# Kernel tuning notes

Measured on AMD Instinct MI355X. Metric: run time of the kernel, lower is better.

Reference implementation:

```python
import jax, jax.numpy as jnp
import numpy as np

HID, HEADS, FF, DEPTH = 1152, 16, 4304, 2
HD = HID // HEADS            # 72
ROT = HD // 2                # 36 (rotary_pos_emb width)
S, NSEG = 2048, 4
EPS = 1e-6


def _layernorm(x, w, b):
    m = jnp.mean(x, axis=-1, keepdims=True)
    xc = x - m
    v = jnp.mean(xc * xc, axis=-1, keepdims=True)
    return xc * jax.lax.rsqrt(v + EPS) * w + b


def _rotate_half(x):
    x1, x2 = jnp.split(x, 2, axis=-1)
    return jnp.concatenate([-x2, x1], axis=-1)


def _apply_rotary(t, freqs):
    # t: [S, H, D], freqs: [S, D/2]
    emb = jnp.concatenate([freqs, freqs], axis=-1)          # [S, D]
    cos = jnp.cos(emb)[:, None, :]
    sin = jnp.sin(emb)[:, None, :]
    return t * cos + _rotate_half(t) * sin


def setup_inputs() -> dict:
    key = jax.random.key(0)
    ks = jax.random.split(key, 16)
    sd = 0.02
    # rotary freqs as in VisionRotaryEmbedding(dim=HD//2): h-pos and w-pos halves
    inv_freq = 1.0 / (10000.0 ** (jnp.arange(0, ROT, 2, dtype=jnp.float32) / ROT))  # [18]
    pos = jnp.arange(S, dtype=jnp.float32)
    hpos, wpos = pos // 32.0, pos % 32.0
    rotary = jnp.concatenate([jnp.outer(hpos, inv_freq), jnp.outer(wpos, inv_freq)], axis=-1)  # [S, 36]
    return {
        "x": jax.random.normal(ks[0], (S, HID), jnp.float32),
        "cu_seqlens": jnp.arange(NSEG + 1, dtype=jnp.int32) * (S // NSEG),
        "rotary_pos_emb": rotary,
        "norm1_w": jnp.ones((DEPTH, HID), jnp.float32),
        "norm1_b": jnp.zeros((DEPTH, HID), jnp.float32),
        "qkv_w": jax.random.normal(ks[1], (DEPTH, 3 * HID, HID), jnp.float32) * sd,
        "qkv_b": jnp.zeros((DEPTH, 3 * HID), jnp.float32),
        "proj_w": jax.random.normal(ks[2], (DEPTH, HID, HID), jnp.float32) * sd,
        "proj_b": jnp.zeros((DEPTH, HID), jnp.float32),
        "norm2_w": jnp.ones((DEPTH, HID), jnp.float32),
        "norm2_b": jnp.zeros((DEPTH, HID), jnp.float32),
        "fc1_w": jax.random.normal(ks[3], (DEPTH, FF, HID), jnp.float32) * sd,
        "fc1_b": jnp.zeros((DEPTH, FF), jnp.float32),
        "fc2_w": jax.random.normal(ks[4], (DEPTH, HID, FF), jnp.float32) * sd,
        "fc2_b": jnp.zeros((DEPTH, HID), jnp.float32),
    }


def _forward(x, cu_seqlens, rotary_pos_emb, norm1_w, norm1_b, qkv_w, qkv_b,
             proj_w, proj_b, norm2_w, norm2_b, fc1_w, fc1_b, fc2_w, fc2_b):
    seq_len = x.shape[0]
    # block-diagonal additive mask from cu_seqlens (same mask the torch loop builds)
    seg = jnp.searchsorted(cu_seqlens, jnp.arange(seq_len, dtype=cu_seqlens.dtype), side="right") - 1
    same = seg[:, None] == seg[None, :]
    bias = jnp.where(same, jnp.float32(0.0), jnp.finfo(jnp.float32).min)  # [S, S]
    scale = 1.0 / np.sqrt(HD)
    for d in range(DEPTH):
        # --- attention ---
        h = _layernorm(x, norm1_w[d], norm1_b[d])
        qkv = (h @ qkv_w[d].T + qkv_b[d]).reshape(seq_len, 3, HEADS, HD)
        q, k, v = qkv[:, 0], qkv[:, 1], qkv[:, 2]           # [S, H, D]
        q = _apply_rotary(q, rotary_pos_emb)
        k = _apply_rotary(k, rotary_pos_emb)
        scores = jnp.einsum("qhd,khd->hqk", q, k) * scale + bias[None]
        probs = jax.nn.softmax(scores.astype(jnp.float32), axis=-1).astype(q.dtype)
        attn = jnp.einsum("hqk,khd->qhd", probs, v).reshape(seq_len, HID)
        x = x + attn @ proj_w[d].T + proj_b[d]
        # --- MLP (gelu tanh approx) ---
        h2 = _layernorm(x, norm2_w[d], norm2_b[d])
        x = x + jax.nn.gelu(h2 @ fc1_w[d].T + fc1_b[d], approximate=True) @ fc2_w[d].T + fc2_b[d]
    return x


def reference(x, cu_seqlens, rotary_pos_emb, norm1_w, norm1_b, qkv_w, qkv_b,
              proj_w, proj_b, norm2_w, norm2_b, fc1_w, fc1_b, fc2_w, fc2_b):
    return _forward(x, cu_seqlens, rotary_pos_emb, norm1_w, norm1_b, qkv_w, qkv_b,
                    proj_w, proj_b, norm2_w, norm2_b, fc1_w, fc1_b, fc2_w, fc2_b)
```

## Files before the change

kernel.cpp:

```cpp
#include <hip/hip_runtime.h>

#define S_LEN 2048
#define HID   1152
#define HEADS 16
#define HD    72
#define ROT   36
#define LD3   3456
#define FF    4304
#define FFP   4320

typedef short s16x8 __attribute__((ext_vector_type(8)));
typedef short s16x4 __attribute__((ext_vector_type(4)));
typedef float f32x4 __attribute__((ext_vector_type(4)));
typedef short bf_t;

__device__ __forceinline__ short f2b(float f) {
  unsigned u = __float_as_uint(f);
  u += 0x7fffu + ((u >> 16) & 1u);
  return (short)(u >> 16);
}
__device__ __forceinline__ float b2f(short h) {
  return __uint_as_float(((unsigned)(unsigned short)h) << 16);
}
__device__ __forceinline__ float gelu_f(float x) {
  float t = tanhf(0.7978845608028654f * (x + 0.044715f * x * x * x));
  return 0.5f * x * (1.0f + t);
}

typedef const __attribute__((address_space(1))) void* gas_p;
typedef __attribute__((address_space(3))) void* las_p;
__device__ __forceinline__ void gload16(const void* g, void* l) {
  __builtin_amdgcn_global_load_lds((gas_p)g, (las_p)l, 16, 0, 0);
}

__global__ __launch_bounds__(256) void convw4_kernel(
    const float* __restrict__ src, int N, int K,
    bf_t* __restrict__ dst, int Kpad)
{
  int idx = blockIdx.x * 256 + threadIdx.x;
  int kq = Kpad >> 2;
  if (idx >= N * kq) return;
  int n = idx / kq, k = (idx % kq) << 2;
  s16x4 o;
  if (k + 3 < K) {
    float4 v = *(const float4*)(src + (size_t)n * K + k);
    o[0] = f2b(v.x); o[1] = f2b(v.y); o[2] = f2b(v.z); o[3] = f2b(v.w);
  } else {
#pragma unroll
    for (int j = 0; j < 4; j++) {
      int kk = k + j;
      o[j] = (kk < K) ? f2b(src[(size_t)n * K + kk]) : (short)0;
    }
  }
  *(s16x4*)(dst + (size_t)n * Kpad + k) = o;
}

__global__ __launch_bounds__(256) void costab_kernel(
    const float* __restrict__ rot, float* __restrict__ ct, float* __restrict__ st)
{
  int i = blockIdx.x * 256 + threadIdx.x;
  if (i < S_LEN * ROT) { float f = rot[i]; ct[i] = cosf(f); st[i] = sinf(f); }
}

__global__ __launch_bounds__(256) void ln_kernel(
    const float* __restrict__ x, const float* __restrict__ wgt,
    const float* __restrict__ bia, bf_t* __restrict__ outb)
{
  const int row = blockIdx.x, tid = threadIdx.x;
  const float4* xr = (const float4*)(x + (size_t)row * HID);
  float4 a = xr[tid];
  float4 b2 = make_float4(0.f, 0.f, 0.f, 0.f);
  const bool has2 = tid < 32;
  if (has2) b2 = xr[256 + tid];
  float s = a.x + a.y + a.z + a.w + b2.x + b2.y + b2.z + b2.w;
  float q = a.x*a.x + a.y*a.y + a.z*a.z + a.w*a.w
          + b2.x*b2.x + b2.y*b2.y + b2.z*b2.z + b2.w*b2.w;
  for (int mk = 32; mk; mk >>= 1) { s += __shfl_xor(s, mk); q += __shfl_xor(q, mk); }
  __shared__ float red[16];
  if ((tid & 63) == 0) { red[tid >> 6] = s; red[8 + (tid >> 6)] = q; }
  __syncthreads();
  if (tid == 0) {
    red[4]  = red[0] + red[1] + red[2] + red[3];
    red[12] = red[8] + red[9] + red[10] + red[11];
  }
  __syncthreads();
  float mean = red[4] * (1.0f / HID);
  float var  = red[12] * (1.0f / HID) - mean * mean;
  float rstd = rsqrtf(var + 1e-6f);
  const float4* w4 = (const float4*)wgt;
  const float4* b4 = (const float4*)bia;
  s16x4* o4 = (s16x4*)(outb + (size_t)row * HID);
  {
    float4 wv = w4[tid], bv = b4[tid];
    s16x4 o;
    o[0] = f2b((a.x - mean) * rstd * wv.x + bv.x);
    o[1] = f2b((a.y - mean) * rstd * wv.y + bv.y);
    o[2] = f2b((a.z - mean) * rstd * wv.z + bv.z);
    o[3] = f2b((a.w - mean) * rstd * wv.w + bv.w);
    o4[tid] = o;
  }
  if (has2) {
    float4 wv = w4[256 + tid], bv = b4[256 + tid];
    s16x4 o;
    o[0] = f2b((b2.x - mean) * rstd * wv.x + bv.x);
    o[1] = f2b((b2.y - mean) * rstd * wv.y + bv.y);
    o[2] = f2b((b2.z - mean) * rstd * wv.z + bv.z);
    o[3] = f2b((b2.w - mean) * rstd * wv.w + bv.w);
    o4[256 + tid] = o;
  }
}

__global__ __launch_bounds__(256) void rotary_kernel(
    bf_t* __restrict__ qkv, const float* __restrict__ ct, const float* __restrict__ st)
{
  int idx = blockIdx.x * 256 + threadIdx.x;
  if (idx >= S_LEN * HEADS * ROT) return;
  int t = idx / (HEADS * ROT);
  int r = idx % (HEADS * ROT);
  int h = r / ROT, dd = r % ROT;
  float c = ct[t * ROT + dd], s = st[t * ROT + dd];
  size_t base = (size_t)t * LD3 + h * HD + dd;
  float q1 = b2f(qkv[base]),        q2 = b2f(qkv[base + ROT]);
  float k1 = b2f(qkv[base + HID]),  k2 = b2f(qkv[base + HID + ROT]);
  const float scale = 0.11785113019775793f;
  qkv[base]             = f2b((q1 * c - q2 * s) * scale);
  qkv[base + ROT]       = f2b((q2 * c + q1 * s) * scale);
  qkv[base + HID]       = f2b(k1 * c - k2 * s);
  qkv[base + HID + ROT] = f2b(k2 * c + k1 * s);
}

template<int MODE>
__global__ __launch_bounds__(256, 4) void gemm_bt(
    const bf_t* __restrict__ A, int lda,
    const bf_t* __restrict__ B, int ldb,
    const float* __restrict__ bias, int nbias,
    void* outp, int ldc, int nvalid, int K, int kchunk)
{
  __shared__ __align__(16) bf_t As[128 * 32];
  __shared__ __align__(16) bf_t Bs[128 * 32];
  const int tid = threadIdx.x;
  const int l = tid & 63, w = tid >> 6;
  const int lr = l & 15, lg = l >> 4;
  const int wm = (w >> 1) * 64, wn = (w & 1) * 64;

  unsigned gx = gridDim.x, gy = gridDim.y, gz = gridDim.z;
  unsigned nwg = gx * gy * gz;
  unsigned lin = (blockIdx.z * gy + blockIdx.y) * gx + blockIdx.x;
  if ((nwg & 7u) == 0u) {
    unsigned q = nwg >> 3;
    lin = (lin & 7u) * q + (lin >> 3);
  }
  const unsigned bz = lin / (gx * gy);
  const unsigned rem = lin % (gx * gy);
  const unsigned by = rem / gx, bx = rem % gx;

  const int rowA0 = by * 128, colB0 = bx * 128;
  const int kb0 = bz * kchunk;
  int kb1 = kb0 + kchunk; if (kb1 > K) kb1 = K;

  const int o1 = tid * 16, o2 = o1 + 4096;
  const int r1 = o1 >> 6, c1 = o1 & 63;
  const int r2 = o2 >> 6, c2 = o2 & 63;
  const char* Ab = (const char*)A;
  const char* Bb = (const char*)B;

  f32x4 acc[4][4] = {};

  for (int kb = kb0; kb < kb1; kb += 32) {
    gload16(Ab + ((size_t)(rowA0 + r1) * lda + kb) * 2 + c1, (char*)As + o1);
    gload16(Ab + ((size_t)(rowA0 + r2) * lda + kb) * 2 + c2, (char*)As + o2);
    gload16(Bb + ((size_t)(colB0 + r1) * ldb + kb) * 2 + c1, (char*)Bs + o1);
    gload16(Bb + ((size_t)(colB0 + r2) * ldb + kb) * 2 + c2, (char*)Bs + o2);
    asm volatile("s_waitcnt vmcnt(0)" ::: "memory");
    __syncthreads();
    s16x8 af[4], bv[4];
#pragma unroll
    for (int mt = 0; mt < 4; mt++) af[mt] = *(const s16x8*)&As[(wm + mt * 16 + lr) * 32 + lg * 8];
#pragma unroll
    for (int nt = 0; nt < 4; nt++) bv[nt] = *(const s16x8*)&Bs[(wn + nt * 16 + lr) * 32 + lg * 8];
#pragma unroll
    for (int mt = 0; mt < 4; mt++)
#pragma unroll
      for (int nt = 0; nt < 4; nt++)
        acc[mt][nt] = __builtin_amdgcn_mfma_f32_16x16x32_bf16(af[mt], bv[nt], acc[mt][nt], 0, 0, 0);
    __syncthreads();
  }

#pragma unroll
  for (int mt = 0; mt < 4; mt++) {
    const int rr = rowA0 + wm + mt * 16 + lg * 4;
#pragma unroll
    for (int nt = 0; nt < 4; nt++) {
      const int cc = colB0 + wn + nt * 16 + lr;
      const float bvl = (cc < nbias) ? bias[cc] : 0.0f;
#pragma unroll
      for (int i = 0; i < 4; i++) {
        float v = acc[mt][nt][i] + bvl;
        const int row = rr + i;
        if (MODE == 0) {
          ((bf_t*)outp)[(size_t)row * ldc + cc] = f2b(v);
        } else if (MODE == 2) {
          if (cc < nvalid)      ((bf_t*)outp)[(size_t)row * ldc + cc] = f2b(gelu_f(v));
          else if (cc < ldc)    ((bf_t*)outp)[(size_t)row * ldc + cc] = 0;
        } else {
          float* P = (float*)outp + (size_t)bz * ((size_t)S_LEN * ldc);
          P[(size_t)row * ldc + cc] = v;
        }
      }
    }
  }
}

__global__ __launch_bounds__(256) void reduce_kernel(
    const float* __restrict__ part, const float* __restrict__ bias,
    const float* __restrict__ resid, float* __restrict__ outp)
{
  int idx = blockIdx.x * 256 + threadIdx.x;
  if (idx >= S_LEN * HID / 4) return;
  float4 r = ((const float4*)resid)[idx];
  float4 bv = ((const float4*)bias)[idx % (HID / 4)];
  float sx = r.x + bv.x, sy = r.y + bv.y, sz = r.z + bv.z, sw = r.w + bv.w;
#pragma unroll
  for (int p = 0; p < 4; p++) {
    float4 v = ((const float4*)(part + (size_t)p * S_LEN * HID))[idx];
    sx += v.x; sy += v.y; sz += v.z; sw += v.w;
  }
  ((float4*)outp)[idx] = make_float4(sx, sy, sz, sw);
}

#define QSTR 104
#define VSTR 72
#define PSTR 72
__global__ __launch_bounds__(256, 2) void attn_kernel(
    const bf_t* __restrict__ qkv, const int* __restrict__ cu, int nseg,
    bf_t* __restrict__ outb)
{
  __shared__ __align__(16) bf_t Qs[64 * QSTR];
  __shared__ __align__(16) bf_t Ks[64 * QSTR];
  __shared__ __align__(16) bf_t VTs[80 * VSTR];
  __shared__ __align__(16) bf_t Pb[4][16 * PSTR];
  const int tid = threadIdx.x;
  const int l = tid & 63, w = tid >> 6;
  const int lr = l & 15, lg = l >> 4;
  const int h = blockIdx.y;
  const int qbase = blockIdx.x * 64;

  int kstart = 0, kend = S_LEN;
  for (int s2 = 0; s2 < nseg; s2++) {
    int a = cu[s2], b = cu[s2 + 1];
    if (qbase >= a && qbase < b) { kstart = a; kend = b; }
  }

  for (int i = tid; i < 64 * QSTR; i += 256)
    if ((i % QSTR) >= HD) { Qs[i] = 0; Ks[i] = 0; }
  for (int i = tid; i < 80 * VSTR; i += 256)
    if ((i / VSTR) >= HD) VTs[i] = 0;
  for (int c = tid; c < 576; c += 256) {
    int r = c / 9, j = c % 9;
    *(s16x8*)&Qs[r * QSTR + j * 8] =
        *(const s16x8*)&qkv[(size_t)(qbase + r) * LD3 + h * HD + j * 8];
  }
  __syncthreads();
  s16x8 qf[3];
#pragma unroll
  for (int ks = 0; ks < 3; ks++)
    qf[ks] = *(const s16x8*)&Qs[(w * 16 + lr) * QSTR + ks * 32 + lg * 8];

  float m_i[4], l_i[4];
  f32x4 Of[5] = {};
#pragma unroll
  for (int i = 0; i < 4; i++) { m_i[i] = -1e30f; l_i[i] = 0.0f; }

  for (int kb = kstart; kb < kend; kb += 64) {
    __syncthreads();
    for (int c = tid; c < 576; c += 256) {
      int r = c / 9, j = c % 9;
      int gr = kb + r; if (gr >= kend) gr = kend - 1;
      *(s16x8*)&Ks[r * QSTR + j * 8] =
          *(const s16x8*)&qkv[(size_t)gr * LD3 + HID + h * HD + j * 8];
    }
    for (int c = tid; c < 576; c += 256) {
      int r = c / 9, j = c % 9;
      int gr = kb + r; if (gr >= kend) gr = kend - 1;
      s16x8 v = *(const s16x8*)&qkv[(size_t)gr * LD3 + 2 * HID + h * HD + j * 8];
#pragma unroll
      for (int jj = 0; jj < 8; jj++) VTs[(j * 8 + jj) * VSTR + r] = v[jj];
    }
    __syncthreads();

    f32x4 sc[4] = {};
#pragma unroll
    for (int kc = 0; kc < 4; kc++) {
#pragma unroll
      for (int ks = 0; ks < 3; ks++) {
        s16x8 kf = *(const s16x8*)&Ks[(kc * 16 + lr) * QSTR + ks * 32 + lg * 8];
        sc[kc] = __builtin_amdgcn_mfma_f32_16x16x32_bf16(qf[ks], kf, sc[kc], 0, 0, 0);
      }
    }
#pragma unroll
    for (int kc = 0; kc < 4; kc++) {
      if ((kb + kc * 16 + lr) >= kend) {
#pragma unroll
        for (int i = 0; i < 4; i++) sc[kc][i] = -1e30f;
      }
    }
    float tmax[4], scl[4], rs[4];
#pragma unroll
    for (int i = 0; i < 4; i++) {
      float t = fmaxf(fmaxf(sc[0][i], sc[1][i]), fmaxf(sc[2][i], sc[3][i]));
#pragma unroll
      for (int d2 = 1; d2 < 16; d2 <<= 1) t = fmaxf(t, __shfl_xor(t, d2));
      tmax[i] = t;
    }
#pragma unroll
    for (int i = 0; i < 4; i++) {
      float mn = fmaxf(m_i[i], tmax[i]);
      scl[i] = __expf(m_i[i] - mn);
      m_i[i] = mn;
      rs[i] = 0.0f;
    }
#pragma unroll
    for (int kc = 0; kc < 4; kc++)
#pragma unroll
      for (int i = 0; i < 4; i++) {
        float p = __expf(sc[kc][i] - m_i[i]);
        sc[kc][i] = p;
        rs[i] += p;
      }
#pragma unroll
    for (int i = 0; i < 4; i++) {
#pragma unroll
      for (int d2 = 1; d2 < 16; d2 <<= 1) rs[i] += __shfl_xor(rs[i], d2);
      l_i[i] = l_i[i] * scl[i] + rs[i];
    }
#pragma unroll
    for (int nt = 0; nt < 5; nt++)
#pragma unroll
      for (int i = 0; i < 4; i++) Of[nt][i] *= scl[i];
#pragma unroll
    for (int kc = 0; kc < 4; kc++)
#pragma unroll
      for (int i = 0; i < 4; i++)
        Pb[w][(lg * 4 + i) * PSTR + kc * 16 + lr] = f2b(sc[kc][i]);
    __syncthreads();
    s16x8 pf[2];
#pragma unroll
    for (int k2 = 0; k2 < 2; k2++)
      pf[k2] = *(const s16x8*)&Pb[w][lr * PSTR + k2 * 32 + lg * 8];
#pragma unroll
    for (int nt = 0; nt < 5; nt++) {
#pragma unroll
      for (int k2 = 0; k2 < 2; k2++) {
        s16x8 vf = *(const s16x8*)&VTs[(nt * 16 + lr) * VSTR + k2 * 32 + lg * 8];
        Of[nt] = __builtin_amdgcn_mfma_f32_16x16x32_bf16(pf[k2], vf, Of[nt], 0, 0, 0);
      }
    }
  }
  float inv[4];
#pragma unroll
  for (int i = 0; i < 4; i++) inv[i] = 1.0f / l_i[i];
#pragma unroll
  for (int nt = 0; nt < 5; nt++) {
    int cc = nt * 16 + lr;
    if (cc < HD) {
#pragma unroll
      for (int i = 0; i < 4; i++) {
        int row = qbase + w * 16 + lg * 4 + i;
        outb[(size_t)row * HID + h * HD + cc] = f2b(Of[nt][i] * inv[i]);
      }
    }
  }
}

extern "C" void kernel_launch(void* const* d_in, const int* in_sizes, int n_in,
                              void* d_out, int out_size, void* d_ws, size_t ws_size,
                              hipStream_t stream) {
  const float* x     = (const float*)d_in[0];
  const int*   cu    = (const int*)d_in[1];
  const float* rotab = (const float*)d_in[2];
  const float* n1w   = (const float*)d_in[3];
  const float* n1b   = (const float*)d_in[4];
  const float* qkvw  = (const float*)d_in[5];
  const float* qkvb  = (const float*)d_in[6];
  const float* projw = (const float*)d_in[7];
  const float* projb = (const float*)d_in[8];
  const float* n2w   = (const float*)d_in[9];
  const float* n2b   = (const float*)d_in[10];
  const float* fc1w  = (const float*)d_in[11];
  const float* fc1b  = (const float*)d_in[12];
  const float* fc2w  = (const float*)d_in[13];
  const float* fc2b  = (const float*)d_in[14];
  float* out = (float*)d_out;
  char* ws = (char*)d_ws;

  size_t off = 0;
  float* xbuf = (float*)(ws + off); off += (size_t)S_LEN * HID * 4;
  bf_t* hbf   = (bf_t*)(ws + off);  off += (size_t)S_LEN * HID * 2;
  bf_t* qkvbf = (bf_t*)(ws + off);
  bf_t* ff1bf = (bf_t*)(ws + off);  off += (size_t)S_LEN * FFP * 2;
  bf_t* attnbf= (bf_t*)(ws + off);  off += (size_t)S_LEN * HID * 2;
  bf_t* wslot = (bf_t*)(ws + off);  off += (size_t)4352 * 1152 * 2;
  float* ctab = (float*)(ws + off); off += (size_t)S_LEN * ROT * 4;
  float* stab = (float*)(ws + off); off += (size_t)S_LEN * ROT * 4;
  float* part = (float*)(ws + off); off += (size_t)4 * S_LEN * HID * 4;

  hipMemcpyAsync(xbuf, x, (size_t)S_LEN * HID * 4, hipMemcpyDeviceToDevice, stream);
  costab_kernel<<<(S_LEN * ROT + 255) / 256, 256, 0, stream>>>(rotab, ctab, stab);

  const int nseg = in_sizes[1] - 1;
  const int RED_GRID = (S_LEN * HID / 4 + 255) / 256;

  for (int d = 0; d < 2; d++) {
    ln_kernel<<<S_LEN, 256, 0, stream>>>(xbuf, n1w + d * HID, n1b + d * HID, hbf);
    convw4_kernel<<<(LD3 * HID / 4 + 255) / 256, 256, 0, stream>>>(
        qkvw + (size_t)d * LD3 * HID, LD3, HID, wslot, HID);
    gemm_bt<0><<<dim3(LD3 / 128, 16), 256, 0, stream>>>(
        hbf, HID, wslot, HID, qkvb + (size_t)d * LD3, LD3, qkvbf, LD3, LD3, HID, HID);
    rotary_kernel<<<(S_LEN * HEADS * ROT + 255) / 256, 256, 0, stream>>>(qkvbf, ctab, stab);
    attn_kernel<<<dim3(S_LEN / 64, HEADS), 256, 0, stream>>>(qkvbf, cu, nseg, attnbf);
    convw4_kernel<<<(HID * HID / 4 + 255) / 256, 256, 0, stream>>>(
        projw + (size_t)d * HID * HID, HID, HID, wslot, HID);
    gemm_bt<3><<<dim3(HID / 128, 16, 4), 256, 0, stream>>>(
        attnbf, HID, wslot, HID, nullptr, 0, part, HID, HID, HID, 288);
    reduce_kernel<<<RED_GRID, 256, 0, stream>>>(part, projb + (size_t)d * HID, xbuf, xbuf);
    ln_kernel<<<S_LEN, 256, 0, stream>>>(xbuf, n2w + d * HID, n2b + d * HID, hbf);
    convw4_kernel<<<(FF * HID / 4 + 255) / 256, 256, 0, stream>>>(
        fc1w + (size_t)d * FF * HID, FF, HID, wslot, HID);
    gemm_bt<2><<<dim3(4352 / 128, 16), 256, 0, stream>>>(
        hbf, HID, wslot, HID, fc1b + (size_t)d * FF, FF, ff1bf, FFP, FF, HID, HID);
    convw4_kernel<<<(HID * FFP / 4 + 255) / 256, 256, 0, stream>>>(
        fc2w + (size_t)d * HID * FF, HID, FF, wslot, FFP);
    gemm_bt<3><<<dim3(HID / 128, 16, 4), 256, 0, stream>>>(
        ff1bf, FFP, wslot, FFP, nullptr, 0, part, HID, HID, FFP, 1088);
    float* outp = (d == 1) ? out : xbuf;
    reduce_kernel<<<RED_GRID, 256, 0, stream>>>(part, fc2b + (size_t)d * HID, xbuf, outp);
  }
}
```

Baseline: 461.4 us.

## Double-buffer GEMM shared tiles and shrink N tile to 64

```diff
diff --git a/kernel.cpp b/kernel.cpp
--- a/kernel.cpp
+++ b/kernel.cpp
@@ -136,12 +136,12 @@
     const float* __restrict__ bias, int nbias,
     void* outp, int ldc, int nvalid, int K, int kchunk)
 {
-  __shared__ __align__(16) bf_t As[128 * 32];
-  __shared__ __align__(16) bf_t Bs[128 * 32];
+  __shared__ __align__(16) bf_t As[2][128 * 32];
+  __shared__ __align__(16) bf_t Bs[2][64 * 32];
   const int tid = threadIdx.x;
   const int l = tid & 63, w = tid >> 6;
   const int lr = l & 15, lg = l >> 4;
-  const int wm = (w >> 1) * 64, wn = (w & 1) * 64;
+  const int wm = (w >> 1) * 64, wn = (w & 1) * 32;
 
   unsigned gx = gridDim.x, gy = gridDim.y, gz = gridDim.z;
   unsigned nwg = gx * gy * gz;
@@ -154,43 +154,60 @@
   const unsigned rem = lin % (gx * gy);
   const unsigned by = rem / gx, bx = rem % gx;
 
-  const int rowA0 = by * 128, colB0 = bx * 128;
+  const int rowA0 = by * 128, colB0 = bx * 64;
   const int kb0 = bz * kchunk;
   int kb1 = kb0 + kchunk; if (kb1 > K) kb1 = K;
 
-  const int o1 = tid * 16, o2 = o1 + 4096;
-  const int r1 = o1 >> 6, c1 = o1 & 63;
-  const int r2 = o2 >> 6, c2 = o2 & 63;
+  const int oA1 = tid * 16, oA2 = oA1 + 4096;
+  const int rA1 = oA1 >> 6, cA1 = oA1 & 63;
+  const int rA2 = rA1 + 64;
+  const int oB = tid * 16;
+  const int rB = oB >> 6, cB = oB & 63;
   const char* Ab = (const char*)A;
   const char* Bb = (const char*)B;
 
-  f32x4 acc[4][4] = {};
-
+#define STAGE(buf, kk) do { \
+    gload16(Ab + ((size_t)(rowA0 + rA1) * lda + (kk)) * 2 + cA1, (char*)As[buf] + oA1); \
+    gload16(Ab + ((size_t)(rowA0 + rA2) * lda + (kk)) * 2 + cA1, (char*)As[buf] + oA2); \
+    gload16(Bb + ((size_t)(colB0 + rB)  * ldb + (kk)) * 2 + cB,  (char*)Bs[buf] + oB);  \
+  } while (0)
+
+  f32x4 acc[4][2] = {};
+
+  STAGE(0, kb0);
+  asm volatile("s_waitcnt vmcnt(0)" ::: "memory");
+  __builtin_amdgcn_s_barrier();
+  __builtin_amdgcn_sched_barrier(0);
+
+  int cur = 0;
   for (int kb = kb0; kb < kb1; kb += 32) {
-    gload16(Ab + ((size_t)(rowA0 + r1) * lda + kb) * 2 + c1, (char*)As + o1);
-    gload16(Ab + ((size_t)(rowA0 + r2) * lda + kb) * 2 + c2, (char*)As + o2);
-    gload16(Bb + ((size_t)(colB0 + r1) * ldb + kb) * 2 + c1, (char*)Bs + o1);
-    gload16(Bb + ((size_t)(colB0 + r2) * ldb + kb) * 2 + c2, (char*)Bs + o2);
+    if (kb + 32 < kb1) STAGE(cur ^ 1, kb + 32);
+    s16x8 af[4], bv[2];
+#pragma unroll
+    for (int mt = 0; mt < 4; mt++)
+      af[mt] = *(const s16x8*)&As[cur][(wm + mt * 16 + lr) * 32 + lg * 8];
+#pragma unroll
+    for (int nt = 0; nt < 2; nt++)
+      bv[nt] = *(const s16x8*)&Bs[cur][(wn + nt * 16 + lr) * 32 + lg * 8];
+    asm volatile("s_waitcnt lgkmcnt(0)" ::: "memory");
+    __builtin_amdgcn_sched_barrier(0);
+#pragma unroll
+    for (int mt = 0; mt < 4; mt++)
+#pragma unroll
+      for (int nt = 0; nt < 2; nt++)
+        acc[mt][nt] = __builtin_amdgcn_mfma_f32_16x16x32_bf16(af[mt], bv[nt], acc[mt][nt], 0, 0, 0);
     asm volatile("s_waitcnt vmcnt(0)" ::: "memory");
-    __syncthreads();
-    s16x8 af[4], bv[4];
-#pragma unroll
-    for (int mt = 0; mt < 4; mt++) af[mt] = *(const s16x8*)&As[(wm + mt * 16 + lr) * 32 + lg * 8];
-#pragma unroll
-    for (int nt = 0; nt < 4; nt++) bv[nt] = *(const s16x8*)&Bs[(wn + nt * 16 + lr) * 32 + lg * 8];
-#pragma unroll
-    for (int mt = 0; mt < 4; mt++)
-#pragma unroll
-      for (int nt = 0; nt < 4; nt++)
-        acc[mt][nt] = __builtin_amdgcn_mfma_f32_16x16x32_bf16(af[mt], bv[nt], acc[mt][nt], 0, 0, 0);
-    __syncthreads();
-  }
+    __builtin_amdgcn_s_barrier();
+    __builtin_amdgcn_sched_barrier(0);
+    cur ^= 1;
+  }
+#undef STAGE
 
 #pragma unroll
   for (int mt = 0; mt < 4; mt++) {
     const int rr = rowA0 + wm + mt * 16 + lg * 4;
 #pragma unroll
-    for (int nt = 0; nt < 4; nt++) {
+    for (int nt = 0; nt < 2; nt++) {
       const int cc = colB0 + wn + nt * 16 + lr;
       const float bvl = (cc < nbias) ? bias[cc] : 0.0f;
 #pragma unroll
@@ -414,23 +431,23 @@
     ln_kernel<<<S_LEN, 256, 0, stream>>>(xbuf, n1w + d * HID, n1b + d * HID, hbf);
     convw4_kernel<<<(LD3 * HID / 4 + 255) / 256, 256, 0, stream>>>(
         qkvw + (size_t)d * LD3 * HID, LD3, HID, wslot, HID);
-    gemm_bt<0><<<dim3(LD3 / 128, 16), 256, 0, stream>>>(
+    gemm_bt<0><<<dim3(LD3 / 64, 16), 256, 0, stream>>>(
         hbf, HID, wslot, HID, qkvb + (size_t)d * LD3, LD3, qkvbf, LD3, LD3, HID, HID);
     rotary_kernel<<<(S_LEN * HEADS * ROT + 255) / 256, 256, 0, stream>>>(qkvbf, ctab, stab);
     attn_kernel<<<dim3(S_LEN / 64, HEADS), 256, 0, stream>>>(qkvbf, cu, nseg, attnbf);
     convw4_kernel<<<(HID * HID / 4 + 255) / 256, 256, 0, stream>>>(
         projw + (size_t)d * HID * HID, HID, HID, wslot, HID);
-    gemm_bt<3><<<dim3(HID / 128, 16, 4), 256, 0, stream>>>(
+    gemm_bt<3><<<dim3(HID / 64, 16, 4), 256, 0, stream>>>(
         attnbf, HID, wslot, HID, nullptr, 0, part, HID, HID, HID, 288);
     reduce_kernel<<<RED_GRID, 256, 0, stream>>>(part, projb + (size_t)d * HID, xbuf, xbuf);
     ln_kernel<<<S_LEN, 256, 0, stream>>>(xbuf, n2w + d * HID, n2b + d * HID, hbf);
     convw4_kernel<<<(FF * HID / 4 + 255) / 256, 256, 0, stream>>>(
         fc1w + (size_t)d * FF * HID, FF, HID, wslot, HID);
-    gemm_bt<2><<<dim3(4352 / 128, 16), 256, 0, stream>>>(
+    gemm_bt<2><<<dim3(4352 / 64, 16), 256, 0, stream>>>(
         hbf, HID, wslot, HID, fc1b + (size_t)d * FF, FF, ff1bf, FFP, FF, HID, HID);
     convw4_kernel<<<(HID * FFP / 4 + 255) / 256, 256, 0, stream>>>(
         fc2w + (size_t)d * HID * FF, HID, FF, wslot, FFP);
-    gemm_bt<3><<<dim3(HID / 128, 16, 4), 256, 0, stream>>>(
+    gemm_bt<3><<<dim3(HID / 64, 16, 4), 256, 0, stream>>>(
         ff1bf, FFP, wslot, FFP, nullptr, 0, part, HID, HID, FFP, 1088);
     float* outp = (d == 1) ? out : xbuf;
     reduce_kernel<<<RED_GRID, 256, 0, stream>>>(part, fc2b + (size_t)d * HID, xbuf, outp);
```

New measurement: 469.6 us. Within noise of the previous version (+1.8%).
